# Kernel tuning notes

Hardware: AMD Instinct MI355X
Metric: run time of the kernel (lower is better)

Reference implementation:

```python
import jax, jax.numpy as jnp
import numpy as np

N = 20000
E = 320000
F_IN = 50
HID = 64          # hidden_channels
HEADS = 8
WIDTH = HID * HEADS  # 512
NUM_CLASSES = 121


def setup_inputs() -> dict:
    key = jax.random.key(0)
    ks = jax.random.split(key, 16)
    def p(k, shape, fan_in):
        return (jax.random.normal(k, shape, dtype=jnp.float32) / np.sqrt(fan_in)).astype(jnp.float32)
    x = jax.random.normal(ks[0], (N, F_IN), dtype=jnp.float32)
    edge_index = jax.random.randint(ks[1], (2, E), 0, N, dtype=jnp.int64)
    return {
        "x": x,
        "edge_index": edge_index,
        # layer 1: 50 -> 64, heads=8, concat
        "W1": p(ks[2], (F_IN, HEADS * HID), F_IN),
        "a1_src": p(ks[3], (HEADS, HID), HID),
        "a1_dst": p(ks[4], (HEADS, HID), HID),
        "b1": jnp.zeros((HEADS * HID,), jnp.float32),
        # layer 2: 512 -> 512, heads=1, concat
        "W2": p(ks[5], (WIDTH, WIDTH), WIDTH),
        "a2_src": p(ks[6], (1, WIDTH), WIDTH),
        "a2_dst": p(ks[7], (1, WIDTH), WIDTH),
        "b2": jnp.zeros((WIDTH,), jnp.float32),
        # layer 3: 512 -> 121, heads=1, concat=False (mean)
        "W3": p(ks[8], (WIDTH, NUM_CLASSES), WIDTH),
        "a3_src": p(ks[9], (1, NUM_CLASSES), NUM_CLASSES),
        "a3_dst": p(ks[10], (1, NUM_CLASSES), NUM_CLASSES),
        "b3": jnp.zeros((NUM_CLASSES,), jnp.float32),
    }


def gat_conv(x, src, dst, W, a_src, a_dst, b, heads, out_ch, concat):
    n = x.shape[0]
    h = (x @ W).reshape(n, heads, out_ch)                 # [N, H, C]
    al_s = jnp.sum(h * a_src, axis=-1)                     # [N, H]
    al_d = jnp.sum(h * a_dst, axis=-1)                     # [N, H]
    e = jax.nn.leaky_relu(al_s[src] + al_d[dst], 0.2)      # [E, H]
    # edge softmax per destination node (stable)
    m = jax.ops.segment_max(e, dst, num_segments=n)        # [N, H]
    m = jnp.where(jnp.isfinite(m), m, 0.0)
    ex = jnp.exp(e - m[dst])
    z = jax.ops.segment_sum(ex, dst, num_segments=n)       # [N, H]
    alpha = ex / (z[dst] + 1e-16)                          # [E, H]
    msg = h[src] * alpha[..., None]                        # [E, H, C]
    out = jax.ops.segment_sum(msg, dst, num_segments=n)    # [N, H, C]
    out = out.reshape(n, heads * out_ch) if concat else out.mean(axis=1)
    return out + b


def reference(x, edge_index, W1, a1_src, a1_dst, b1, W2, a2_src, a2_dst, b2, W3, a3_src, a3_dst, b3):
    n = x.shape[0]
    # PyG GATConv adds self loops by default
    loops = jnp.arange(n, dtype=edge_index.dtype)
    src = jnp.concatenate([edge_index[0], loops])
    dst = jnp.concatenate([edge_index[1], loops])
    # eval mode: dropout is identity
    x1 = gat_conv(x, src, dst, W1, a1_src, a1_dst, b1, HEADS, HID, True)
    h = jax.nn.elu(x1)
    x1 = gat_conv(h, src, dst, W2, a2_src, a2_dst, b2, 1, WIDTH, True)
    h = jax.nn.elu(x1)
    x1 = gat_conv(h, src, dst, W3, a3_src, a3_dst, b3, 1, NUM_CLASSES, False)
    return x1
```

## Files before the change

kernel.cpp:

```cpp
#include <hip/hip_runtime.h>
#include <hip/hip_bf16.h>
#include <hip/hip_fp16.h>

#define NN     20000
#define ERAW   320000
#define ETOT   (ERAW + NN)
#define F_IN   50
#define HID    64
#define HEADS  8
#define WIDTH  512
#define NCLS   121
#define NCLS_P 128

typedef __attribute__((ext_vector_type(8))) __bf16 bf16x8;
typedef __attribute__((ext_vector_type(4))) float floatx4;

__device__ __forceinline__ unsigned short f32_to_bf16_rn(float f) {
  unsigned u = __float_as_uint(f);
  unsigned r = u + 0x7fffu + ((u >> 16) & 1u);
  return (unsigned short)(r >> 16);
}
__device__ __forceinline__ void split_one(float f, unsigned short& h,
                                          unsigned short& l) {
  h = f32_to_bf16_rn(f);
  float fh = __uint_as_float(((unsigned)h) << 16);
  l = f32_to_bf16_rn(f - fh);
}

__device__ __forceinline__ float2 u2f2(unsigned u) {
  __half2 hv = *reinterpret_cast<__half2*>(&u);
  return __half22float2(hv);
}

#define PW_BLOCKS 449
__global__ __launch_bounds__(256) void prep_weights(
    const float* __restrict__ W1, const float* __restrict__ W2,
    const float* __restrict__ W3, const float* __restrict__ a1s,
    const float* __restrict__ a1d, unsigned short* __restrict__ w1hHi,
    unsigned short* __restrict__ w1hLo, unsigned short* __restrict__ w2tHi,
    unsigned short* __restrict__ w2tLo, unsigned short* __restrict__ w3tHi,
    unsigned short* __restrict__ w3tLo, float* __restrict__ w1as,
    float* __restrict__ w1ad) {
  __shared__ float t[32][33];
  const int b = blockIdx.x;
  if (b < 320) {
    const float* W;
    unsigned short *thi, *tlo;
    int M, Mp, bx, by;
    const int K = WIDTH;
    if (b < 256) {
      W = W2; thi = w2tHi; tlo = w2tLo; M = WIDTH; Mp = WIDTH;
      bx = b & 15; by = b >> 4;
    } else {
      int bb = b - 256;
      W = W3; thi = w3tHi; tlo = w3tLo; M = NCLS; Mp = NCLS_P;
      bx = bb & 15; by = bb >> 4;
    }
    int k0 = bx * 32, m0 = by * 32;
    int tx = threadIdx.x & 31, ty = threadIdx.x >> 5;
    #pragma unroll
    for (int r = 0; r < 4; ++r) {
      int k = k0 + ty + r * 8, m = m0 + tx;
      float v = 0.f;
      if (k < K && m < M) v = W[(size_t)k * M + m];
      t[ty + r * 8][tx] = v;
    }
    __syncthreads();
    #pragma unroll
    for (int r = 0; r < 4; ++r) {
      int m = m0 + ty + r * 8, k = k0 + tx;
      if (m < Mp && k < K) {
        unsigned short h, l;
        split_one(t[tx][ty + r * 8], h, l);
        thi[(size_t)m * K + k] = h;
        tlo[(size_t)m * K + k] = l;
      }
    }
  } else if (b < 448) {
    int idx = (b - 320) * 256 + threadIdx.x;
    if (idx < HEADS * HID * HID) {
      int hd = idx >> 12, rem = idx & 4095;
      int col = rem >> 6, k = rem & 63;
      float v = (k < F_IN) ? W1[(size_t)k * WIDTH + hd * HID + col] : 0.f;
      unsigned short h, l;
      split_one(v, h, l);
      w1hHi[idx] = h;
      w1hLo[idx] = l;
    }
  } else {
    for (int idx = threadIdx.x; idx < 2 * F_IN * HEADS; idx += 256) {
      int which = idx >= F_IN * HEADS;
      int r = which ? idx - F_IN * HEADS : idx;
      int k = r >> 3, h = r & 7;
      const float* a = which ? a1d : a1s;
      float s = 0.f;
      for (int c = 0; c < HID; ++c)
        s += W1[(size_t)k * WIDTH + h * HID + c] * a[h * HID + c];
      (which ? w1ad : w1as)[r] = s;
    }
  }
}

__global__ __launch_bounds__(256) void gemm_mfma_split(
    const unsigned short* __restrict__ Ahi, const unsigned short* __restrict__ Alo,
    const unsigned short* __restrict__ Bthi, const unsigned short* __restrict__ Btlo,
    __half* __restrict__ C16, int N, int K, int M, int Mp) {
  __shared__ unsigned short sAhi[4096], sAlo[4096], sBhi[4096], sBlo[4096];
  const int tid = threadIdx.x;
  const int wave = tid >> 6, lane = tid & 63;
  const int wr = wave >> 1, wc = wave & 1;
  const int r0 = blockIdx.y * 128;
  const int c0 = blockIdx.x * 128;
  const int lkg = lane >> 4;
  const int lmn = lane & 15;

  const int skg = tid & 3;
  const int srow = tid >> 2;
  int ra0 = r0 + srow;        if (ra0 > NN - 1) ra0 = NN - 1;
  int ra1 = r0 + srow + 64;   if (ra1 > NN - 1) ra1 = NN - 1;
  const unsigned short* gAhi0 = Ahi + (size_t)ra0 * K + skg * 8;
  const unsigned short* gAhi1 = Ahi + (size_t)ra1 * K + skg * 8;
  const unsigned short* gAlo0 = Alo + (size_t)ra0 * K + skg * 8;
  const unsigned short* gAlo1 = Alo + (size_t)ra1 * K + skg * 8;
  const unsigned short* gBhi0 = Bthi + (size_t)(c0 + srow) * K + skg * 8;
  const unsigned short* gBhi1 = Bthi + (size_t)(c0 + srow + 64) * K + skg * 8;
  const unsigned short* gBlo0 = Btlo + (size_t)(c0 + srow) * K + skg * 8;
  const unsigned short* gBlo1 = Btlo + (size_t)(c0 + srow + 64) * K + skg * 8;

  floatx4 acc[4][4] = {};

  uint4 a0, a1, a2, a3, b0, b1, b2, b3;
  auto gload = [&](int kk) {
    a0 = *(const uint4*)(gAhi0 + kk);
    a1 = *(const uint4*)(gAhi1 + kk);
    a2 = *(const uint4*)(gAlo0 + kk);
    a3 = *(const uint4*)(gAlo1 + kk);
    b0 = *(const uint4*)(gBhi0 + kk);
    b1 = *(const uint4*)(gBhi1 + kk);
    b2 = *(const uint4*)(gBlo0 + kk);
    b3 = *(const uint4*)(gBlo1 + kk);
  };
  gload(0);

  const int w0 = (skg * 128 + srow) * 8;
  const int w1 = (skg * 128 + srow + 64) * 8;

  for (int k0 = 0; k0 < K; k0 += 32) {
    __syncthreads();
    *(uint4*)(sAhi + w0) = a0;
    *(uint4*)(sAhi + w1) = a1;
    *(uint4*)(sAlo + w0) = a2;
    *(uint4*)(sAlo + w1) = a3;
    *(uint4*)(sBhi + w0) = b0;
    *(uint4*)(sBhi + w1) = b1;
    *(uint4*)(sBlo + w0) = b2;
    *(uint4*)(sBlo + w1) = b3;
    __syncthreads();
    if (k0 + 32 < K) gload(k0 + 32);

    bf16x8 fAhi[4], fAlo[4], fBhi[4], fBlo[4];
    #pragma unroll
    for (int mi = 0; mi < 4; ++mi) {
      int m = wr * 64 + mi * 16 + lmn;
      fAhi[mi] = *(const bf16x8*)(sAhi + (lkg * 128 + m) * 8);
      fAlo[mi] = *(const bf16x8*)(sAlo + (lkg * 128 + m) * 8);
    }
    #pragma unroll
    for (int ni = 0; ni < 4; ++ni) {
      int n = wc * 64 + ni * 16 + lmn;
      fBhi[ni] = *(const bf16x8*)(sBhi + (lkg * 128 + n) * 8);
      fBlo[ni] = *(const bf16x8*)(sBlo + (lkg * 128 + n) * 8);
    }
    #pragma unroll
    for (int mi = 0; mi < 4; ++mi)
      #pragma unroll
      for (int ni = 0; ni < 4; ++ni) {
        acc[mi][ni] = __builtin_amdgcn_mfma_f32_16x16x32_bf16(
            fAhi[mi], fBhi[ni], acc[mi][ni], 0, 0, 0);
        acc[mi][ni] = __builtin_amdgcn_mfma_f32_16x16x32_bf16(
            fAhi[mi], fBlo[ni], acc[mi][ni], 0, 0, 0);
        acc[mi][ni] = __builtin_amdgcn_mfma_f32_16x16x32_bf16(
            fAlo[mi], fBhi[ni], acc[mi][ni], 0, 0, 0);
      }
  }

  #pragma unroll
  for (int mi = 0; mi < 4; ++mi) {
    #pragma unroll
    for (int r = 0; r < 4; ++r) {
      int grow = r0 + wr * 64 + mi * 16 + (lane >> 4) * 4 + r;
      if (grow >= N) continue;
      #pragma unroll
      for (int ni = 0; ni < 4; ++ni) {
        int gcol = c0 + wc * 64 + ni * 16 + lmn;
        if (gcol < Mp) {
          float v = (gcol < M) ? acc[mi][ni][r] : 0.f;
          C16[(size_t)grow * Mp + gcol] = __float2half(v);
        }
      }
    }
  }
}

__global__ __launch_bounds__(256) void gemm_l1_heads(
    const unsigned short* __restrict__ Ahi, const unsigned short* __restrict__ Alo,
    const unsigned short* __restrict__ Bthi, const unsigned short* __restrict__ Btlo,
    unsigned short* __restrict__ outHi, unsigned short* __restrict__ outLo,
    const float* __restrict__ bias) {
  __shared__ unsigned short sAhi[8192], sAlo[8192], sBhi[4096], sBlo[4096];
  const int tid = threadIdx.x;
  const int wave = tid >> 6, lane = tid & 63;
  const int r0 = blockIdx.x * 128;
  const int hd = blockIdx.y;
  const int lkg = lane >> 4, lmn = lane & 15;

  #pragma unroll
  for (int t = 0; t < 4; ++t) {
    int cid = tid + t * 256;
    int row = cid >> 3, c = cid & 7;
    int gr = r0 + row; if (gr > NN - 1) gr = NN - 1;
    const size_t goff = (size_t)gr * WIDTH + hd * HID + c * 8;
    int loff = (((c >> 2) * 4 + (c & 3)) * 128 + row) * 8;
    *(uint4*)(sAhi + loff) = *(const uint4*)(Ahi + goff);
    *(uint4*)(sAlo + loff) = *(const uint4*)(Alo + goff);
  }
  #pragma unroll
  for (int t = 0; t < 2; ++t) {
    int cid = tid + t * 256;
    int col = cid >> 3, c = cid & 7;
    const size_t goff = (size_t)(hd * HID + col) * HID + c * 8;
    int loff = (((c >> 2) * 4 + (c & 3)) * 64 + col) * 8;
    *(uint4*)(sBhi + loff) = *(const uint4*)(Bthi + goff);
    *(uint4*)(sBlo + loff) = *(const uint4*)(Btlo + goff);
  }
  __syncthreads();

  floatx4 acc[2][4] = {};
  #pragma unroll
  for (int ks = 0; ks < 2; ++ks) {
    bf16x8 fAhi[2], fAlo[2], fBhi[4], fBlo[4];
    #pragma unroll
    for (int mi = 0; mi < 2; ++mi) {
      int m = wave * 32 + mi * 16 + lmn;
      int off = ((ks * 4 + lkg) * 128 + m) * 8;
      fAhi[mi] = *(const bf16x8*)(sAhi + off);
      fAlo[mi] = *(const bf16x8*)(sAlo + off);
    }
    #pragma unroll
    for (int ni = 0; ni < 4; ++ni) {
      int n = ni * 16 + lmn;
      int off = ((ks * 4 + lkg) * 64 + n) * 8;
      fBhi[ni] = *(const bf16x8*)(sBhi + off);
      fBlo[ni] = *(const bf16x8*)(sBlo + off);
    }
    #pragma unroll
    for (int mi = 0; mi < 2; ++mi)
      #pragma unroll
      for (int ni = 0; ni < 4; ++ni) {
        acc[mi][ni] = __builtin_amdgcn_mfma_f32_16x16x32_bf16(
            fAhi[mi], fBhi[ni], acc[mi][ni], 0, 0, 0);
        acc[mi][ni] = __builtin_amdgcn_mfma_f32_16x16x32_bf16(
            fAhi[mi], fBlo[ni], acc[mi][ni], 0, 0, 0);
        acc[mi][ni] = __builtin_amdgcn_mfma_f32_16x16x32_bf16(
            fAlo[mi], fBhi[ni], acc[mi][ni], 0, 0, 0);
      }
  }

  #pragma unroll
  for (int mi = 0; mi < 2; ++mi) {
    #pragma unroll
    for (int r = 0; r < 4; ++r) {
      int grow = r0 + wave * 32 + mi * 16 + (lane >> 4) * 4 + r;
      if (grow >= NN) continue;
      #pragma unroll
      for (int ni = 0; ni < 4; ++ni) {
        int gcol = hd * HID + ni * 16 + lmn;
        float v = acc[mi][ni][r] + bias[gcol];
        v = (v > 0.f) ? v : (__expf(v) - 1.0f);
        unsigned short hh, ll;
        split_one(v, hh, ll);
        outHi[(size_t)grow * WIDTH + gcol] = hh;
        outLo[(size_t)grow * WIDTH + gcol] = ll;
      }
    }
  }
}

__global__ __launch_bounds__(256) void al1_kernel(
    const float* __restrict__ x, const float* __restrict__ w1as,
    const float* __restrict__ w1ad, float* __restrict__ al_s,
    float* __restrict__ al_d) {
  int n = (blockIdx.x * blockDim.x + threadIdx.x) >> 6;
  int lane = threadIdx.x & 63;
  if (n >= NN) return;
  float xv = (lane < F_IN) ? x[(size_t)n * F_IN + lane] : 0.f;
  float ws[HEADS], wd[HEADS];
  #pragma unroll
  for (int h = 0; h < HEADS; ++h) {
    ws[h] = (lane < F_IN) ? w1as[lane * HEADS + h] : 0.f;
    wd[h] = (lane < F_IN) ? w1ad[lane * HEADS + h] : 0.f;
  }
  #pragma unroll
  for (int h = 0; h < HEADS; ++h) {
    float ss = xv * ws[h], sd = xv * wd[h];
    #pragma unroll
    for (int o = 32; o; o >>= 1) {
      ss += __shfl_xor(ss, o);
      sd += __shfl_xor(sd, o);
    }
    if (lane == 0) {
      al_s[n * HEADS + h] = ss;
      al_d[n * HEADS + h] = sd;
    }
  }
}

template <int C, int CS>
__global__ __launch_bounds__(256) void compute_al16(
    const __half* __restrict__ h16, const float* __restrict__ a_src,
    const float* __restrict__ a_dst, float* __restrict__ al_s,
    float* __restrict__ al_d) {
  int n = (blockIdx.x * blockDim.x + threadIdx.x) >> 6;
  int lane = threadIdx.x & 63;
  if (n >= NN) return;
  const __half* hr = h16 + (size_t)n * CS;
  float ss = 0.f, sd = 0.f;
  if (C % 512 == 0) {
    uint4 raw = *(const uint4*)(hr + lane * 8);
    float f[8];
    float2 t;
    t = u2f2(raw.x); f[0] = t.x; f[1] = t.y;
    t = u2f2(raw.y); f[2] = t.x; f[3] = t.y;
    t = u2f2(raw.z); f[4] = t.x; f[5] = t.y;
    t = u2f2(raw.w); f[6] = t.x; f[7] = t.y;
    #pragma unroll
    for (int j = 0; j < 8; ++j) {
      int c = lane * 8 + j;
      ss += f[j] * a_src[c];
      sd += f[j] * a_dst[c];
    }
  } else {
    for (int c = lane; c < C; c += 64) {
      float v = __half2float(hr[c]);
      ss += v * a_src[c];
      sd += v * a_dst[c];
    }
  }
  #pragma unroll
  for (int o = 32; o; o >>= 1) {
    ss += __shfl_xor(ss, o);
    sd += __shfl_xor(sd, o);
  }
  if (lane == 0) {
    al_s[n] = ss;
    al_d[n] = sd;
  }
}

__global__ __launch_bounds__(256) void count_deg(
    const int* __restrict__ edst, int* __restrict__ deg) {
  int e = blockIdx.x * blockDim.x + threadIdx.x;
  if (e >= ETOT) return;
  int d = (e < ERAW) ? edst[e] : (e - ERAW);
  atomicAdd(&deg[d], 1);
}

__global__ __launch_bounds__(256) void scan_deg(
    const int* __restrict__ deg, int* __restrict__ rowptr) {
  __shared__ int part[256];
  const int t = threadIdx.x;
  const int CHUNK = (NN + 255) / 256;
  int lo = t * CHUNK, hi = min(lo + CHUNK, NN);
  int s = 0;
  for (int i = lo; i < hi; ++i) s += deg[i];
  part[t] = s;
  __syncthreads();
  for (int off = 1; off < 256; off <<= 1) {
    int v = (t >= off) ? part[t - off] : 0;
    __syncthreads();
    part[t] += v;
    __syncthreads();
  }
  int base = (t == 0) ? 0 : part[t - 1];
  for (int i = lo; i < hi; ++i) {
    rowptr[i] = base;
    base += deg[i];
  }
  if (t == 255) rowptr[NN] = part[255];
}

__global__ __launch_bounds__(256) void scatter_csr(
    const int* __restrict__ esrc, const int* __restrict__ edst,
    const int* __restrict__ rowptr, int* __restrict__ cnt,
    int* __restrict__ csrc) {
  int e = blockIdx.x * blockDim.x + threadIdx.x;
  if (e >= ETOT) return;
  int s, d;
  if (e < ERAW) { s = esrc[e]; d = edst[e]; }
  else          { s = e - ERAW; d = e - ERAW; }
  int pos = rowptr[d] + atomicAdd(&cnt[d], 1);
  csrc[pos] = s;
}

__global__ __launch_bounds__(256) void agg_x_sm(
    const int* __restrict__ rowptr, const int* __restrict__ csrc,
    const float* __restrict__ al_s, const float* __restrict__ al_d,
    const float* __restrict__ x, unsigned short* __restrict__ outHi,
    unsigned short* __restrict__ outLo) {
  const int w = threadIdx.x >> 6, lane = threadIdx.x & 63;
  const int d = blockIdx.x * 4 + w;
  if (d >= NN) return;
  const int r0 = rowptr[d], r1 = rowptr[d + 1];
  const int mh = lane & 7;
  const float ald_my = al_d[d * HEADS + mh];
  float m_my = al_s[d * HEADS + mh] + ald_my;
  m_my = (m_my > 0.f) ? m_my : 0.2f * m_my;

  float z_my = 0.f;
  float acc[HEADS];
  #pragma unroll
  for (int hh = 0; hh < HEADS; ++hh) acc[hh] = 0.f;
  for (int p = r0; p < r1; ++p) {
    int s = csrc[p];
    float v = al_s[s * HEADS + mh] + ald_my;
    v = (v > 0.f) ? v : 0.2f * v;
    float a = __expf(v - m_my);
    z_my += a;
    float xv = (lane < F_IN) ? x[(size_t)s * F_IN + lane] : 0.f;
    #pragma unroll
    for (int hh = 0; hh < HEADS; ++hh) acc[hh] += __shfl(a, hh, 8) * xv;
  }
  #pragma unroll
  for (int hh = 0; hh < HEADS; ++hh) {
    float zh = __shfl(z_my, hh, 8);
    float v = (lane < F_IN) ? acc[hh] / (zh + 1e-16f) : 0.f;
    unsigned short h2, l2;
    split_one(v, h2, l2);
    outHi[(size_t)d * WIDTH + hh * HID + lane] = h2;
    outLo[(size_t)d * WIDTH + hh * HID + lane] = l2;
  }
}

template <int M, int MS, bool ELU, bool SPLIT>
__global__ __launch_bounds__(256) void pull_agg_sm(
    const int* __restrict__ rowptr, const int* __restrict__ csrc,
    const float* __restrict__ al_s, const float* __restrict__ al_d,
    const __half* __restrict__ h16, const float* __restrict__ bias,
    float* __restrict__ out, unsigned short* __restrict__ outHi,
    unsigned short* __restrict__ outLo) {
  constexpr int EPL = MS / 64;
  const int w = threadIdx.x >> 6;
  const int lane = threadIdx.x & 63;
  const int d = blockIdx.x * 4 + w;
  if (d >= NN) return;
  const int r0 = rowptr[d], r1 = rowptr[d + 1];
  const float ald = al_d[d];
  float m = al_s[d] + ald;
  m = (m > 0.f) ? m : 0.2f * m;

  const int base = lane * EPL;
  float acc[EPL];
  #pragma unroll
  for (int j = 0; j < EPL; ++j) acc[j] = 0.f;
  float z = 0.f;

  for (int p = r0; p < r1; ++p) {
    int s = csrc[p];
    float v = al_s[s] + ald;
    v = (v > 0.f) ? v : 0.2f * v;
    float a = __expf(v - m);
    z += a;
    const __half* hr = h16 + (size_t)s * MS + base;
    if (EPL == 8) {
      uint4 raw = *(const uint4*)hr;
      float2 f0 = u2f2(raw.x), f1 = u2f2(raw.y);
      float2 f2 = u2f2(raw.z), f3 = u2f2(raw.w);
      acc[0] += f0.x * a; acc[1] += f0.y * a;
      acc[2] += f1.x * a; acc[3] += f1.y * a;
      acc[4] += f2.x * a; acc[5] += f2.y * a;
      acc[6] += f3.x * a; acc[7] += f3.y * a;
    } else if (EPL == 2) {
      unsigned raw = *(const unsigned*)hr;
      float2 f0 = u2f2(raw);
      acc[0] += f0.x * a;
      acc[1] += f0.y * a;
    } else {
      #pragma unroll
      for (int j = 0; j < EPL; ++j) acc[j] += __half2float(hr[j]) * a;
    }
  }
  const float iz = 1.0f / (z + 1e-16f);

  #pragma unroll
  for (int j = 0; j < EPL; ++j) {
    if ((M == MS) || (base + j < M)) {
      float v = acc[j] * iz + bias[base + j];
      if (ELU) v = (v > 0.f) ? v : (__expf(v) - 1.0f);
      if (SPLIT) {
        unsigned short hh, ll;
        split_one(v, hh, ll);
        outHi[(size_t)d * M + base + j] = hh;
        outLo[(size_t)d * M + base + j] = ll;
      } else {
        out[(size_t)d * M + base + j] = v;
      }
    }
  }
}

extern "C" void kernel_launch(void* const* d_in, const int* in_sizes, int n_in,
                              void* d_out, int out_size, void* d_ws,
                              size_t ws_size, hipStream_t stream) {
  const float* x      = (const float*)d_in[0];
  const int*   ei     = (const int*)d_in[1];
  const float* W1     = (const float*)d_in[2];
  const float* a1_src = (const float*)d_in[3];
  const float* a1_dst = (const float*)d_in[4];
  const float* b1     = (const float*)d_in[5];
  const float* W2     = (const float*)d_in[6];
  const float* a2_src = (const float*)d_in[7];
  const float* a2_dst = (const float*)d_in[8];
  const float* b2     = (const float*)d_in[9];
  const float* W3     = (const float*)d_in[10];
  const float* a3_src = (const float*)d_in[11];
  const float* a3_dst = (const float*)d_in[12];
  const float* b3     = (const float*)d_in[13];
  float* out = (float*)d_out;

  const int* esrc = ei;
  const int* edst = ei + ERAW;

  unsigned short* p1Hi  = (unsigned short*)d_ws;
  unsigned short* p1Lo  = p1Hi + (size_t)NN * WIDTH;
  unsigned short* p2Hi  = p1Lo + (size_t)NN * WIDTH;
  unsigned short* p2Lo  = p2Hi + (size_t)NN * WIDTH;
  __half*        h16    = (__half*)(p2Lo + (size_t)NN * WIDTH);
  unsigned short* w1hHi = (unsigned short*)(h16 + (size_t)NN * WIDTH);
  unsigned short* w1hLo = w1hHi + (size_t)HEADS * HID * HID;
  unsigned short* w2tHi = w1hLo + (size_t)HEADS * HID * HID;
  unsigned short* w2tLo = w2tHi + (size_t)WIDTH * WIDTH;
  unsigned short* w3tHi = w2tLo + (size_t)WIDTH * WIDTH;
  unsigned short* w3tLo = w3tHi + (size_t)NCLS_P * WIDTH;
  float* al_s   = (float*)(w3tLo + (size_t)NCLS_P * WIDTH);
  float* al_d   = al_s + (size_t)NN * HEADS;
  float* w1as   = al_d + (size_t)NN * HEADS;
  float* w1ad   = w1as + F_IN * HEADS;
  int* deg      = (int*)(w1ad + F_IN * HEADS);
  int* cnt      = deg + NN;
  int* rowptr   = cnt + NN;
  int* csrc     = rowptr + NN + 4;

  hipMemsetAsync(deg, 0, (size_t)(2 * NN) * sizeof(int), stream);
  const int eblk = (ETOT + 255) / 256;
  count_deg<<<eblk, 256, 0, stream>>>(edst, deg);
  scan_deg<<<1, 256, 0, stream>>>(deg, rowptr);
  scatter_csr<<<eblk, 256, 0, stream>>>(esrc, edst, rowptr, cnt, csrc);

  prep_weights<<<PW_BLOCKS, 256, 0, stream>>>(
      W1, W2, W3, a1_src, a1_dst, w1hHi, w1hLo, w2tHi, w2tLo, w3tHi, w3tLo,
      w1as, w1ad);

  const int nwblk = (NN + 3) / 4;

  al1_kernel<<<nwblk, 256, 0, stream>>>(x, w1as, w1ad, al_s, al_d);
  agg_x_sm<<<nwblk, 256, 0, stream>>>(rowptr, csrc, al_s, al_d, x, p1Hi,
                                      p1Lo);
  gemm_l1_heads<<<dim3((NN + 127) / 128, HEADS), 256, 0, stream>>>(
      p1Hi, p1Lo, w1hHi, w1hLo, p2Hi, p2Lo, b1);

  gemm_mfma_split<<<dim3(WIDTH / 128, (NN + 127) / 128), 256, 0, stream>>>(
      p2Hi, p2Lo, w2tHi, w2tLo, h16, NN, WIDTH, WIDTH, WIDTH);
  compute_al16<WIDTH, WIDTH><<<nwblk, 256, 0, stream>>>(h16, a2_src, a2_dst,
                                                        al_s, al_d);
  pull_agg_sm<WIDTH, WIDTH, true, true><<<nwblk, 256, 0, stream>>>(
      rowptr, csrc, al_s, al_d, h16, b2, nullptr, p1Hi, p1Lo);

  gemm_mfma_split<<<dim3(NCLS_P / 128, (NN + 127) / 128), 256, 0, stream>>>(
      p1Hi, p1Lo, w3tHi, w3tLo, h16, NN, WIDTH, NCLS, NCLS_P);
  compute_al16<NCLS, NCLS_P><<<nwblk, 256, 0, stream>>>(h16, a3_src, a3_dst,
                                                        al_s, al_d);
  pull_agg_sm<NCLS, NCLS_P, false, false><<<nwblk, 256, 0, stream>>>(
      rowptr, csrc, al_s, al_d, h16, b3, out, nullptr, nullptr);
}
```

Measured before the change: 446.6 us.

## Rewrite split-bf16 GEMM with direct-to-LDS double buffering, 64x64 tiles, XCD-aware mapping

Replaces the 128x128 register-staged split-precision GEMM with a 64x64-tile version. Global tiles are loaded straight into LDS through global_load_lds and double-buffered, so the next K-slice is fetched while the current one feeds the MFMAs. The LDS layout is XOR-swizzled to avoid bank conflicts, and a 1-D grid maps row blocks across the 8 XCDs so neighbouring blocks share cached weight tiles. Smaller tiles raise block count and occupancy but lower MFMA reuse per LDS byte, and the new kernel relies on its hand-written vmcnt waits for correctness.

```diff
diff --git a/kernel.cpp b/kernel.cpp
--- a/kernel.cpp
+++ b/kernel.cpp
@@ -30,6 +30,13 @@
 __device__ __forceinline__ float2 u2f2(unsigned u) {
   __half2 hv = *reinterpret_cast<__half2*>(&u);
   return __half22float2(hv);
+}
+
+__device__ __forceinline__ void gll16(const unsigned short* g,
+                                      const unsigned short* l) {
+  __builtin_amdgcn_global_load_lds(
+      (const __attribute__((address_space(1))) unsigned int*)(const void*)g,
+      (__attribute__((address_space(3))) unsigned int*)(void*)l, 16, 0, 0);
 }
 
 #define PW_BLOCKS 449
@@ -101,102 +108,102 @@
   }
 }
 
-__global__ __launch_bounds__(256) void gemm_mfma_split(
+__global__ __launch_bounds__(256) void gemm_split_db(
     const unsigned short* __restrict__ Ahi, const unsigned short* __restrict__ Alo,
     const unsigned short* __restrict__ Bthi, const unsigned short* __restrict__ Btlo,
-    __half* __restrict__ C16, int N, int K, int M, int Mp) {
-  __shared__ unsigned short sAhi[4096], sAlo[4096], sBhi[4096], sBlo[4096];
+    __half* __restrict__ C16, int N, int K, int M, int Mp, int RB, int CB) {
+  __shared__ unsigned short lds[16384];
+
+  const int f = blockIdx.x;
+  const int xcd = f & 7;
+  const int g = f >> 3;
+  const int cb = g % CB;
+  const int rb = (g / CB) * 8 + xcd;
+  if (rb >= RB) return;
+  const int r0 = rb * 64, c0 = cb * 64;
+
   const int tid = threadIdx.x;
   const int wave = tid >> 6, lane = tid & 63;
   const int wr = wave >> 1, wc = wave & 1;
-  const int r0 = blockIdx.y * 128;
-  const int c0 = blockIdx.x * 128;
-  const int lkg = lane >> 4;
-  const int lmn = lane & 15;
-
-  const int skg = tid & 3;
-  const int srow = tid >> 2;
-  int ra0 = r0 + srow;        if (ra0 > NN - 1) ra0 = NN - 1;
-  int ra1 = r0 + srow + 64;   if (ra1 > NN - 1) ra1 = NN - 1;
-  const unsigned short* gAhi0 = Ahi + (size_t)ra0 * K + skg * 8;
-  const unsigned short* gAhi1 = Ahi + (size_t)ra1 * K + skg * 8;
-  const unsigned short* gAlo0 = Alo + (size_t)ra0 * K + skg * 8;
-  const unsigned short* gAlo1 = Alo + (size_t)ra1 * K + skg * 8;
-  const unsigned short* gBhi0 = Bthi + (size_t)(c0 + srow) * K + skg * 8;
-  const unsigned short* gBhi1 = Bthi + (size_t)(c0 + srow + 64) * K + skg * 8;
-  const unsigned short* gBlo0 = Btlo + (size_t)(c0 + srow) * K + skg * 8;
-  const unsigned short* gBlo1 = Btlo + (size_t)(c0 + srow + 64) * K + skg * 8;
-
-  floatx4 acc[4][4] = {};
-
-  uint4 a0, a1, a2, a3, b0, b1, b2, b3;
-  auto gload = [&](int kk) {
-    a0 = *(const uint4*)(gAhi0 + kk);
-    a1 = *(const uint4*)(gAhi1 + kk);
-    a2 = *(const uint4*)(gAlo0 + kk);
-    a3 = *(const uint4*)(gAlo1 + kk);
-    b0 = *(const uint4*)(gBhi0 + kk);
-    b1 = *(const uint4*)(gBhi1 + kk);
-    b2 = *(const uint4*)(gBlo0 + kk);
-    b3 = *(const uint4*)(gBlo1 + kk);
-  };
-  gload(0);
-
-  const int w0 = (skg * 128 + srow) * 8;
-  const int w1 = (skg * 128 + srow + 64) * 8;
-
-  for (int k0 = 0; k0 < K; k0 += 32) {
+  const int lkg = lane >> 4, lmn = lane & 15;
+
+  const unsigned short* gsrc[4];
+  int ldsoff[4];
+  #pragma unroll
+  for (int j = 0; j < 4; ++j) {
+    int d = wave * 4 + j;
+    int isB = (d >= 8) ? 1 : 0;
+    int dd = d - isB * 8;
+    int arr = dd >> 2, kg = dd & 3;
+    int row = lane ^ (kg * 2);
+    const unsigned short* base;
+    size_t roff;
+    if (!isB) {
+      int ra = r0 + row;
+      if (ra > N - 1) ra = N - 1;
+      base = arr ? Alo : Ahi;
+      roff = (size_t)ra * K;
+    } else {
+      base = arr ? Btlo : Bthi;
+      roff = (size_t)(c0 + row) * K;
+    }
+    gsrc[j] = base + roff + kg * 8;
+    ldsoff[j] = isB * 4096 + arr * 2048 + kg * 512;
+  }
+
+  const int xr = lkg * 2;
+  const int offA = lkg * 512 + ((wr * 32 + lmn) ^ xr) * 8;
+  const int offB = 4096 + lkg * 512 + ((wc * 32 + lmn) ^ xr) * 8;
+
+  floatx4 acc[2][2] = {};
+
+  #pragma unroll
+  for (int j = 0; j < 4; ++j) gll16(gsrc[j], lds + ldsoff[j]);
+
+  const int nk = K >> 5;
+  for (int t = 0; t < nk; ++t) {
+    asm volatile("s_waitcnt vmcnt(0)" ::: "memory");
     __syncthreads();
-    *(uint4*)(sAhi + w0) = a0;
-    *(uint4*)(sAhi + w1) = a1;
-    *(uint4*)(sAlo + w0) = a2;
-    *(uint4*)(sAlo + w1) = a3;
-    *(uint4*)(sBhi + w0) = b0;
-    *(uint4*)(sBhi + w1) = b1;
-    *(uint4*)(sBlo + w0) = b2;
-    *(uint4*)(sBlo + w1) = b3;
-    __syncthreads();
-    if (k0 + 32 < K) gload(k0 + 32);
-
-    bf16x8 fAhi[4], fAlo[4], fBhi[4], fBlo[4];
-    #pragma unroll
-    for (int mi = 0; mi < 4; ++mi) {
-      int m = wr * 64 + mi * 16 + lmn;
-      fAhi[mi] = *(const bf16x8*)(sAhi + (lkg * 128 + m) * 8);
-      fAlo[mi] = *(const bf16x8*)(sAlo + (lkg * 128 + m) * 8);
-    }
-    #pragma unroll
-    for (int ni = 0; ni < 4; ++ni) {
-      int n = wc * 64 + ni * 16 + lmn;
-      fBhi[ni] = *(const bf16x8*)(sBhi + (lkg * 128 + n) * 8);
-      fBlo[ni] = *(const bf16x8*)(sBlo + (lkg * 128 + n) * 8);
-    }
-    #pragma unroll
-    for (int mi = 0; mi < 4; ++mi)
+    if (t + 1 < nk) {
+      const unsigned short* dst = lds + ((t + 1) & 1) * 8192;
       #pragma unroll
-      for (int ni = 0; ni < 4; ++ni) {
-        acc[mi][ni] = __builtin_amdgcn_mfma_f32_16x16x32_bf16(
-            fAhi[mi], fBhi[ni], acc[mi][ni], 0, 0, 0);
-        acc[mi][ni] = __builtin_amdgcn_mfma_f32_16x16x32_bf16(
-            fAhi[mi], fBlo[ni], acc[mi][ni], 0, 0, 0);
-        acc[mi][ni] = __builtin_amdgcn_mfma_f32_16x16x32_bf16(
-            fAlo[mi], fBhi[ni], acc[mi][ni], 0, 0, 0);
-      }
-  }
-
-  #pragma unroll
-  for (int mi = 0; mi < 4; ++mi) {
+      for (int j = 0; j < 4; ++j)
+        gll16(gsrc[j] + (t + 1) * 32, dst + ldsoff[j]);
+    }
+    const unsigned short* Lb = lds + (t & 1) * 8192;
+    bf16x8 a0h = *(const bf16x8*)(Lb + offA);
+    bf16x8 a1h = *(const bf16x8*)(Lb + offA + 128);
+    bf16x8 a0l = *(const bf16x8*)(Lb + offA + 2048);
+    bf16x8 a1l = *(const bf16x8*)(Lb + offA + 2048 + 128);
+    bf16x8 b0h = *(const bf16x8*)(Lb + offB);
+    bf16x8 b1h = *(const bf16x8*)(Lb + offB + 128);
+    bf16x8 b0l = *(const bf16x8*)(Lb + offB + 2048);
+    bf16x8 b1l = *(const bf16x8*)(Lb + offB + 2048 + 128);
+    acc[0][0] = __builtin_amdgcn_mfma_f32_16x16x32_bf16(a0h, b0h, acc[0][0], 0, 0, 0);
+    acc[0][0] = __builtin_amdgcn_mfma_f32_16x16x32_bf16(a0h, b0l, acc[0][0], 0, 0, 0);
+    acc[0][0] = __builtin_amdgcn_mfma_f32_16x16x32_bf16(a0l, b0h, acc[0][0], 0, 0, 0);
+    acc[0][1] = __builtin_amdgcn_mfma_f32_16x16x32_bf16(a0h, b1h, acc[0][1], 0, 0, 0);
+    acc[0][1] = __builtin_amdgcn_mfma_f32_16x16x32_bf16(a0h, b1l, acc[0][1], 0, 0, 0);
+    acc[0][1] = __builtin_amdgcn_mfma_f32_16x16x32_bf16(a0l, b1h, acc[0][1], 0, 0, 0);
+    acc[1][0] = __builtin_amdgcn_mfma_f32_16x16x32_bf16(a1h, b0h, acc[1][0], 0, 0, 0);
+    acc[1][0] = __builtin_amdgcn_mfma_f32_16x16x32_bf16(a1h, b0l, acc[1][0], 0, 0, 0);
+    acc[1][0] = __builtin_amdgcn_mfma_f32_16x16x32_bf16(a1l, b0h, acc[1][0], 0, 0, 0);
+    acc[1][1] = __builtin_amdgcn_mfma_f32_16x16x32_bf16(a1h, b1h, acc[1][1], 0, 0, 0);
+    acc[1][1] = __builtin_amdgcn_mfma_f32_16x16x32_bf16(a1h, b1l, acc[1][1], 0, 0, 0);
+    acc[1][1] = __builtin_amdgcn_mfma_f32_16x16x32_bf16(a1l, b1h, acc[1][1], 0, 0, 0);
+  }
+
+  #pragma unroll
+  for (int mi = 0; mi < 2; ++mi) {
     #pragma unroll
     for (int r = 0; r < 4; ++r) {
-      int grow = r0 + wr * 64 + mi * 16 + (lane >> 4) * 4 + r;
+      int grow = r0 + wr * 32 + mi * 16 + (lane >> 4) * 4 + r;
       if (grow >= N) continue;
       #pragma unroll
-      for (int ni = 0; ni < 4; ++ni) {
-        int gcol = c0 + wc * 64 + ni * 16 + lmn;
-        if (gcol < Mp) {
-          float v = (gcol < M) ? acc[mi][ni][r] : 0.f;
-          C16[(size_t)grow * Mp + gcol] = __float2half(v);
-        }
+      for (int ni = 0; ni < 2; ++ni) {
+        int gcol = c0 + wc * 32 + ni * 16 + lmn;
+        float v = (gcol < M) ? acc[mi][ni][r] : 0.f;
+        C16[(size_t)grow * Mp + gcol] = __float2half(v);
       }
     }
   }
@@ -568,15 +575,18 @@
   gemm_l1_heads<<<dim3((NN + 127) / 128, HEADS), 256, 0, stream>>>(
       p1Hi, p1Lo, w1hHi, w1hLo, p2Hi, p2Lo, b1);
 
-  gemm_mfma_split<<<dim3(WIDTH / 128, (NN + 127) / 128), 256, 0, stream>>>(
-      p2Hi, p2Lo, w2tHi, w2tLo, h16, NN, WIDTH, WIDTH, WIDTH);
+  const int RB = (NN + 63) / 64;
+  const int RBG = (RB + 7) / 8;
+
+  gemm_split_db<<<RBG * 8 * (WIDTH / 64), 256, 0, stream>>>(
+      p2Hi, p2Lo, w2tHi, w2tLo, h16, NN, WIDTH, WIDTH, WIDTH, RB, WIDTH / 64);
   compute_al16<WIDTH, WIDTH><<<nwblk, 256, 0, stream>>>(h16, a2_src, a2_dst,
                                                         al_s, al_d);
   pull_agg_sm<WIDTH, WIDTH, true, true><<<nwblk, 256, 0, stream>>>(
       rowptr, csrc, al_s, al_d, h16, b2, nullptr, p1Hi, p1Lo);
 
-  gemm_mfma_split<<<dim3(NCLS_P / 128, (NN + 127) / 128), 256, 0, stream>>>(
-      p1Hi, p1Lo, w3tHi, w3tLo, h16, NN, WIDTH, NCLS, NCLS_P);
+  gemm_split_db<<<RBG * 8 * (NCLS_P / 64), 256, 0, stream>>>(
+      p1Hi, p1Lo, w3tHi, w3tLo, h16, NN, WIDTH, NCLS, NCLS_P, RB, NCLS_P / 64);
   compute_al16<NCLS, NCLS_P><<<nwblk, 256, 0, stream>>>(h16, a3_src, a3_dst,
                                                         al_s, al_d);
   pull_agg_sm<NCLS, NCLS_P, false, false><<<nwblk, 256, 0, stream>>>(
```

Measured after the change: 501.4 us. +12.3%, slower.
